# Kernel tuning notes

Measured on AMD Instinct MI355X. Metric: run time of the kernel, lower is better.

## Reference

```python
import jax, jax.numpy as jnp
import numpy as np

B, L, E, H = 4, 1024, 256, 8
DH = E // H  # head_size = 32


def setup_inputs() -> dict:
    key = jax.random.key(0)
    ks = jax.random.split(key, 12)
    node_features = jax.random.normal(ks[0], (B, L, E), dtype=jnp.float32)
    # sparse-ish adjacency with self loops so no row is all-masked
    adj = jax.random.bernoulli(ks[1], 0.05, (B, L, L))
    adj = adj | jnp.eye(L, dtype=bool)[None]
    key_edge_features = jax.random.normal(ks[2], (B, L, L, DH), dtype=jnp.float32)
    s = 1.0 / np.sqrt(E)
    Wq = jax.random.normal(ks[3], (E, E), dtype=jnp.float32) * s
    bq = jnp.zeros((E,), dtype=jnp.float32)
    Wk = jax.random.normal(ks[4], (E, E), dtype=jnp.float32) * s
    bk = jnp.zeros((E,), dtype=jnp.float32)
    Wv = jax.random.normal(ks[5], (E, E), dtype=jnp.float32) * s
    bv = jnp.zeros((E,), dtype=jnp.float32)
    Wo = jax.random.normal(ks[6], (E, E), dtype=jnp.float32) * s
    bo = jnp.zeros((E,), dtype=jnp.float32)
    return {"node_features": node_features, "batched_adj": adj,
            "key_edge_features": key_edge_features,
            "Wq": Wq, "bq": bq, "Wk": Wk, "bk": bk,
            "Wv": Wv, "bv": bv, "Wo": Wo, "bo": bo}


def _heads(x):
    # (B, L, E) -> (B, H, L, DH)
    b, l, _ = x.shape
    return x.reshape(b, l, H, DH).transpose(0, 2, 1, 3)


def reference(node_features, batched_adj, key_edge_features,
              Wq, bq, Wk, bk, Wv, bv, Wo, bo):
    Q = _heads(node_features @ Wq.T + bq)  # (B,H,L,DH)
    K = _heads(node_features @ Wk.T + bk)
    V = _heads(node_features @ Wv.T + bv)
    scores = jnp.einsum('bhnd,bhmd->bhnm', Q, K)
    scores = scores + jnp.einsum('bhnd,bnmd->bhnm', Q, key_edge_features)
    scores = scores / jnp.sqrt(jnp.asarray(E, dtype=scores.dtype))
    adj = batched_adj[:, None, :, :]  # (B,1,L,L) broadcast over heads
    scores = jnp.where(adj, scores, -jnp.inf)
    probs = jax.nn.softmax(scores, axis=-1)
    probs = jnp.where(jnp.isnan(probs), 0.0, probs)  # rows with no edges -> 0
    out = jnp.einsum('bhnm,bhmd->bhnd', probs, V)  # (B,H,L,DH)
    out = out.transpose(0, 2, 1, 3).reshape(node_features.shape[0], -1, E)
    return out @ Wo.T + bo
```

## Files before the change

### kernel.cpp

```cpp
#include <hip/hip_runtime.h>

#define Bv 4
#define Lv 1024
#define Ev 256
#define Hv 8
#define DHv 32

__global__ __launch_bounds__(256) void gemm_fused(
    const float* __restrict__ A,
    const float* __restrict__ W0, const float* __restrict__ b0, float* __restrict__ C0,
    const float* __restrict__ W1, const float* __restrict__ b1, float* __restrict__ C1,
    const float* __restrict__ W2, const float* __restrict__ b2, float* __restrict__ C2) {
    __shared__ float Xs[32][34];
    __shared__ float Ws[32][68];
    const int g = blockIdx.y >> 2;
    const float* __restrict__ W    = (g == 0) ? W0 : (g == 1) ? W1 : W2;
    const float* __restrict__ bias = (g == 0) ? b0 : (g == 1) ? b1 : b2;
    float* __restrict__ C          = (g == 0) ? C0 : (g == 1) ? C1 : C2;

    const int row0 = blockIdx.x * 32;
    const int col0 = (blockIdx.y & 3) * 64;
    const int t = threadIdx.x;
    const int tx = t & 15, ty = t >> 4;
    const int lr = t >> 3, lk = (t & 7) * 4;

    float acc[2][4] = {};

    for (int k0 = 0; k0 < 256; k0 += 32) {
        const float4 av = *(const float4*)&A[(size_t)(row0 + lr) * 256 + k0 + lk];
        const float4 w0 = *(const float4*)&W[(size_t)(col0 + lr) * 256 + k0 + lk];
        const float4 w1 = *(const float4*)&W[(size_t)(col0 + 32 + lr) * 256 + k0 + lk];
        Xs[lk + 0][lr] = av.x; Xs[lk + 1][lr] = av.y;
        Xs[lk + 2][lr] = av.z; Xs[lk + 3][lr] = av.w;
        Ws[lk + 0][lr] = w0.x; Ws[lk + 1][lr] = w0.y;
        Ws[lk + 2][lr] = w0.z; Ws[lk + 3][lr] = w0.w;
        Ws[lk + 0][32 + lr] = w1.x; Ws[lk + 1][32 + lr] = w1.y;
        Ws[lk + 2][32 + lr] = w1.z; Ws[lk + 3][32 + lr] = w1.w;
        __syncthreads();

        #pragma unroll
        for (int kk = 0; kk < 32; ++kk) {
            const float2 a2 = *(const float2*)&Xs[kk][ty * 2];
            const float4 b4 = *(const float4*)&Ws[kk][tx * 4];
            acc[0][0] = fmaf(a2.x, b4.x, acc[0][0]);
            acc[0][1] = fmaf(a2.x, b4.y, acc[0][1]);
            acc[0][2] = fmaf(a2.x, b4.z, acc[0][2]);
            acc[0][3] = fmaf(a2.x, b4.w, acc[0][3]);
            acc[1][0] = fmaf(a2.y, b4.x, acc[1][0]);
            acc[1][1] = fmaf(a2.y, b4.y, acc[1][1]);
            acc[1][2] = fmaf(a2.y, b4.z, acc[1][2]);
            acc[1][3] = fmaf(a2.y, b4.w, acc[1][3]);
        }
        __syncthreads();
    }

    const float4 bv4 = *(const float4*)&bias[col0 + tx * 4];
    #pragma unroll
    for (int ri = 0; ri < 2; ++ri) {
        const int row = row0 + ty * 2 + ri;
        float4 o;
        o.x = acc[ri][0] + bv4.x; o.y = acc[ri][1] + bv4.y;
        o.z = acc[ri][2] + bv4.z; o.w = acc[ri][3] + bv4.w;
        *(float4*)&C[(size_t)row * 256 + col0 + tx * 4] = o;
    }
}

__global__ __launch_bounds__(256) void attn_sparse(const float* __restrict__ Qb,
                                                   const float* __restrict__ Kb,
                                                   const float* __restrict__ Vb,
                                                   const int* __restrict__ adj,
                                                   const float* __restrict__ KE,
                                                   float* __restrict__ AT) {
    __shared__ __align__(16) float Qs[Ev];
    __shared__ __align__(16) float S[Hv][260];
    __shared__ int idxm[256];
    __shared__ int cntS;
    __shared__ float mh[Hv], lh[Hv], scaleh[Hv];

    const int bid = blockIdx.x;
    const int b = bid >> 10;
    const int n = bid & 1023;
    const int t = threadIdx.x;
    const int lane = t & 63;
    const int h_of_t = t >> 5;
    const size_t nrow = (size_t)(b * Lv + n) * Lv;

    Qs[t] = Qb[(size_t)(b * Lv + n) * Ev + t] * 0.0625f;
    if (t < Hv) { mh[t] = -1e30f; lh[t] = 0.f; }

    float acc = 0.f;
    const float* __restrict__ vcol = Vb + (size_t)b * Lv * Ev + t;
    const float4* __restrict__ K4 = (const float4*)Kb;
    const float4* __restrict__ KE4 = (const float4*)KE;
    const float4* __restrict__ Q4 = (const float4*)Qs;

    for (int c = 0; c < 4; ++c) {
        if (t == 0) cntS = 0;
        __syncthreads();

        const int m = c * 256 + t;
        const bool p = adj[nrow + m] != 0;
        const unsigned long long mask = __ballot(p);
        const int prefix = __popcll(mask & ((1ull << lane) - 1ull));
        int base = 0;
        if (lane == 0) base = atomicAdd(&cntS, __popcll(mask));
        base = __shfl(base, 0, 64);
        if (p) idxm[base + prefix] = m;
        __syncthreads();

        const int cnt = cntS;

        for (int tb = 0; tb < cnt * 8; tb += 256) {
            const int task = tb + t;
            if (task < cnt * 8) {
                const int ei = task >> 3, h = task & 7;
                const int mm = idxm[ei];
                const float4* kp = K4 + (size_t)(b * Lv + mm) * 64 + h * 8;
                const float4* kep = KE4 + (nrow + mm) * 8;
                const float4* qp = Q4 + h * 8;
                float dot = 0.f;
                #pragma unroll
                for (int j = 0; j < 8; ++j) {
                    const float4 kv = kp[j], kf = kep[j], qv = qp[j];
                    dot = fmaf(qv.x, kv.x + kf.x, dot);
                    dot = fmaf(qv.y, kv.y + kf.y, dot);
                    dot = fmaf(qv.z, kv.z + kf.z, dot);
                    dot = fmaf(qv.w, kv.w + kf.w, dot);
                }
                S[h][ei] = dot;
            }
        }
        __syncthreads();

        {
            const int h = t >> 5, d = t & 31;
            float cmax = -1e30f;
            for (int i = d; i < cnt; i += 32) cmax = fmaxf(cmax, S[h][i]);
            #pragma unroll
            for (int off = 16; off >= 1; off >>= 1)
                cmax = fmaxf(cmax, __shfl_xor(cmax, off, 64));
            const float oldm = mh[h];
            const float newm = fmaxf(oldm, cmax);
            float csum = 0.f;
            for (int i = d; i < cnt; i += 32) {
                const float pz = __expf(S[h][i] - newm);
                S[h][i] = pz;
                csum += pz;
            }
            #pragma unroll
            for (int off = 16; off >= 1; off >>= 1)
                csum += __shfl_xor(csum, off, 64);
            if (d == 0) {
                const float sc = __expf(oldm - newm);
                scaleh[h] = sc;
                lh[h] = lh[h] * sc + csum;
                mh[h] = newm;
            }
        }
        __syncthreads();

        {
            acc *= scaleh[h_of_t];
            int i = 0;
            for (; i + 4 <= cnt; i += 4) {
                const int m0 = idxm[i], m1 = idxm[i + 1], m2 = idxm[i + 2], m3 = idxm[i + 3];
                const float p0 = S[h_of_t][i],     p1 = S[h_of_t][i + 1];
                const float p2 = S[h_of_t][i + 2], p3 = S[h_of_t][i + 3];
                const float v0 = vcol[(size_t)m0 * Ev];
                const float v1 = vcol[(size_t)m1 * Ev];
                const float v2 = vcol[(size_t)m2 * Ev];
                const float v3 = vcol[(size_t)m3 * Ev];
                acc = fmaf(p0, v0, acc);
                acc = fmaf(p1, v1, acc);
                acc = fmaf(p2, v2, acc);
                acc = fmaf(p3, v3, acc);
            }
            for (; i < cnt; ++i)
                acc = fmaf(S[h_of_t][i], vcol[(size_t)idxm[i] * Ev], acc);
        }
        __syncthreads();
    }

    AT[(size_t)(b * Lv + n) * Ev + t] = acc / lh[h_of_t];
}

extern "C" void kernel_launch(void* const* d_in, const int* in_sizes, int n_in,
                              void* d_out, int out_size, void* d_ws, size_t ws_size,
                              hipStream_t stream) {
    const float* X   = (const float*)d_in[0];
    const int*   adj = (const int*)d_in[1];
    const float* KE  = (const float*)d_in[2];
    const float* Wq  = (const float*)d_in[3];
    const float* bq  = (const float*)d_in[4];
    const float* Wk  = (const float*)d_in[5];
    const float* bk  = (const float*)d_in[6];
    const float* Wv  = (const float*)d_in[7];
    const float* bv  = (const float*)d_in[8];
    const float* Wo  = (const float*)d_in[9];
    const float* bo  = (const float*)d_in[10];

    const size_t NE = (size_t)Bv * Lv * Ev;
    float* Qb = (float*)d_ws;
    float* Kb = Qb + NE;
    float* Vb = Kb + NE;
    float* AT = Vb + NE;
    float* out = (float*)d_out;

    const dim3 blk(256);

    hipLaunchKernelGGL(gemm_fused, dim3(128, 12), blk, 0, stream, X,
                       Wq, bq, Qb, Wk, bk, Kb, Wv, bv, Vb);
    hipLaunchKernelGGL(attn_sparse, dim3(Bv * Lv), blk, 0, stream,
                       Qb, Kb, Vb, adj, KE, AT);
    hipLaunchKernelGGL(gemm_fused, dim3(128, 4), blk, 0, stream, AT,
                       Wo, bo, out, Wo, bo, out, Wo, bo, out);
}
```

Measured before the change: 723.5 us.

## Replace chunked online softmax with single-pass compaction; enlarge GEMM tiles with swizzle

The attention kernel now compacts all neighbours of a row into shared memory up front, then computes scores, an exact softmax and the PV accumulation once. This replaces the four-chunk online-softmax loop and removes most of its barriers and rescaling. Q for each head is held in registers, and each thread keeps a fixed head. The projection GEMM moves to 64x64 tiles with 4x4 per-thread outputs and XOR-swizzled shared stores, so each block does more work per load. The costs are a larger shared-memory footprint (about 37KB per block), which may lower occupancy, and fewer GEMM blocks.

```diff
diff --git a/kernel.cpp b/kernel.cpp
--- a/kernel.cpp
+++ b/kernel.cpp
@@ -11,56 +11,71 @@
     const float* __restrict__ W0, const float* __restrict__ b0, float* __restrict__ C0,
     const float* __restrict__ W1, const float* __restrict__ b1, float* __restrict__ C1,
     const float* __restrict__ W2, const float* __restrict__ b2, float* __restrict__ C2) {
-    __shared__ float Xs[32][34];
+    __shared__ float Xs[32][68];
     __shared__ float Ws[32][68];
     const int g = blockIdx.y >> 2;
     const float* __restrict__ W    = (g == 0) ? W0 : (g == 1) ? W1 : W2;
     const float* __restrict__ bias = (g == 0) ? b0 : (g == 1) ? b1 : b2;
     float* __restrict__ C          = (g == 0) ? C0 : (g == 1) ? C1 : C2;
 
-    const int row0 = blockIdx.x * 32;
+    const int row0 = blockIdx.x * 64;
     const int col0 = (blockIdx.y & 3) * 64;
     const int t = threadIdx.x;
     const int tx = t & 15, ty = t >> 4;
-    const int lr = t >> 3, lk = (t & 7) * 4;
-
-    float acc[2][4] = {};
+    const int lr = t >> 3;
+    const int lk = (t & 7) * 4;
+    const int xsw = 4 * ((lk >> 3) & 3);
+    const int xa = lr ^ xsw;
+
+    float acc[4][4] = {};
 
     for (int k0 = 0; k0 < 256; k0 += 32) {
-        const float4 av = *(const float4*)&A[(size_t)(row0 + lr) * 256 + k0 + lk];
+        const float4 a0 = *(const float4*)&A[(size_t)(row0 + lr) * 256 + k0 + lk];
+        const float4 a1 = *(const float4*)&A[(size_t)(row0 + 32 + lr) * 256 + k0 + lk];
         const float4 w0 = *(const float4*)&W[(size_t)(col0 + lr) * 256 + k0 + lk];
         const float4 w1 = *(const float4*)&W[(size_t)(col0 + 32 + lr) * 256 + k0 + lk];
-        Xs[lk + 0][lr] = av.x; Xs[lk + 1][lr] = av.y;
-        Xs[lk + 2][lr] = av.z; Xs[lk + 3][lr] = av.w;
-        Ws[lk + 0][lr] = w0.x; Ws[lk + 1][lr] = w0.y;
-        Ws[lk + 2][lr] = w0.z; Ws[lk + 3][lr] = w0.w;
-        Ws[lk + 0][32 + lr] = w1.x; Ws[lk + 1][32 + lr] = w1.y;
-        Ws[lk + 2][32 + lr] = w1.z; Ws[lk + 3][32 + lr] = w1.w;
+        Xs[lk + 0][xa] = a0.x; Xs[lk + 1][xa] = a0.y;
+        Xs[lk + 2][xa] = a0.z; Xs[lk + 3][xa] = a0.w;
+        Xs[lk + 0][32 + xa] = a1.x; Xs[lk + 1][32 + xa] = a1.y;
+        Xs[lk + 2][32 + xa] = a1.z; Xs[lk + 3][32 + xa] = a1.w;
+        Ws[lk + 0][xa] = w0.x; Ws[lk + 1][xa] = w0.y;
+        Ws[lk + 2][xa] = w0.z; Ws[lk + 3][xa] = w0.w;
+        Ws[lk + 0][32 + xa] = w1.x; Ws[lk + 1][32 + xa] = w1.y;
+        Ws[lk + 2][32 + xa] = w1.z; Ws[lk + 3][32 + xa] = w1.w;
         __syncthreads();
 
         #pragma unroll
         for (int kk = 0; kk < 32; ++kk) {
-            const float2 a2 = *(const float2*)&Xs[kk][ty * 2];
-            const float4 b4 = *(const float4*)&Ws[kk][tx * 4];
-            acc[0][0] = fmaf(a2.x, b4.x, acc[0][0]);
-            acc[0][1] = fmaf(a2.x, b4.y, acc[0][1]);
-            acc[0][2] = fmaf(a2.x, b4.z, acc[0][2]);
-            acc[0][3] = fmaf(a2.x, b4.w, acc[0][3]);
-            acc[1][0] = fmaf(a2.y, b4.x, acc[1][0]);
-            acc[1][1] = fmaf(a2.y, b4.y, acc[1][1]);
-            acc[1][2] = fmaf(a2.y, b4.z, acc[1][2]);
-            acc[1][3] = fmaf(a2.y, b4.w, acc[1][3]);
+            const int s = (kk >> 3) & 3;
+            const float4 av = *(const float4*)&Xs[kk][(ty ^ s) * 4];
+            const float4 bv = *(const float4*)&Ws[kk][(tx ^ s) * 4];
+            acc[0][0] = fmaf(av.x, bv.x, acc[0][0]);
+            acc[0][1] = fmaf(av.x, bv.y, acc[0][1]);
+            acc[0][2] = fmaf(av.x, bv.z, acc[0][2]);
+            acc[0][3] = fmaf(av.x, bv.w, acc[0][3]);
+            acc[1][0] = fmaf(av.y, bv.x, acc[1][0]);
+            acc[1][1] = fmaf(av.y, bv.y, acc[1][1]);
+            acc[1][2] = fmaf(av.y, bv.z, acc[1][2]);
+            acc[1][3] = fmaf(av.y, bv.w, acc[1][3]);
+            acc[2][0] = fmaf(av.z, bv.x, acc[2][0]);
+            acc[2][1] = fmaf(av.z, bv.y, acc[2][1]);
+            acc[2][2] = fmaf(av.z, bv.z, acc[2][2]);
+            acc[2][3] = fmaf(av.z, bv.w, acc[2][3]);
+            acc[3][0] = fmaf(av.w, bv.x, acc[3][0]);
+            acc[3][1] = fmaf(av.w, bv.y, acc[3][1]);
+            acc[3][2] = fmaf(av.w, bv.z, acc[3][2]);
+            acc[3][3] = fmaf(av.w, bv.w, acc[3][3]);
         }
         __syncthreads();
     }
 
     const float4 bv4 = *(const float4*)&bias[col0 + tx * 4];
     #pragma unroll
-    for (int ri = 0; ri < 2; ++ri) {
-        const int row = row0 + ty * 2 + ri;
+    for (int r = 0; r < 4; ++r) {
+        const int row = row0 + ty * 4 + r;
         float4 o;
-        o.x = acc[ri][0] + bv4.x; o.y = acc[ri][1] + bv4.y;
-        o.z = acc[ri][2] + bv4.z; o.w = acc[ri][3] + bv4.w;
+        o.x = acc[r][0] + bv4.x; o.y = acc[r][1] + bv4.y;
+        o.z = acc[r][2] + bv4.z; o.w = acc[r][3] + bv4.w;
         *(float4*)&C[(size_t)row * 256 + col0 + tx * 4] = o;
     }
 }
@@ -71,117 +86,106 @@
                                                    const int* __restrict__ adj,
                                                    const float* __restrict__ KE,
                                                    float* __restrict__ AT) {
-    __shared__ __align__(16) float Qs[Ev];
-    __shared__ __align__(16) float S[Hv][260];
-    __shared__ int idxm[256];
-    __shared__ int cntS;
-    __shared__ float mh[Hv], lh[Hv], scaleh[Hv];
+    __shared__ float Qs[Hv][36];
+    __shared__ float S[Hv][1028];
+    __shared__ int idxm[Lv];
+    __shared__ int cnt_s;
+    __shared__ float lh[Hv];
 
     const int bid = blockIdx.x;
     const int b = bid >> 10;
     const int n = bid & 1023;
     const int t = threadIdx.x;
     const int lane = t & 63;
-    const int h_of_t = t >> 5;
     const size_t nrow = (size_t)(b * Lv + n) * Lv;
 
-    Qs[t] = Qb[(size_t)(b * Lv + n) * Ev + t] * 0.0625f;
-    if (t < Hv) { mh[t] = -1e30f; lh[t] = 0.f; }
-
-    float acc = 0.f;
-    const float* __restrict__ vcol = Vb + (size_t)b * Lv * Ev + t;
-    const float4* __restrict__ K4 = (const float4*)Kb;
-    const float4* __restrict__ KE4 = (const float4*)KE;
-    const float4* __restrict__ Q4 = (const float4*)Qs;
-
+    Qs[t >> 5][t & 31] = Qb[(size_t)(b * Lv + n) * Ev + t] * 0.0625f;
+    if (t == 0) cnt_s = 0;
+    __syncthreads();
+
+    #pragma unroll
     for (int c = 0; c < 4; ++c) {
-        if (t == 0) cntS = 0;
-        __syncthreads();
-
         const int m = c * 256 + t;
         const bool p = adj[nrow + m] != 0;
         const unsigned long long mask = __ballot(p);
         const int prefix = __popcll(mask & ((1ull << lane) - 1ull));
         int base = 0;
-        if (lane == 0) base = atomicAdd(&cntS, __popcll(mask));
+        if (lane == 0) base = atomicAdd(&cnt_s, __popcll(mask));
         base = __shfl(base, 0, 64);
         if (p) idxm[base + prefix] = m;
-        __syncthreads();
-
-        const int cnt = cntS;
-
-        for (int tb = 0; tb < cnt * 8; tb += 256) {
-            const int task = tb + t;
-            if (task < cnt * 8) {
-                const int ei = task >> 3, h = task & 7;
-                const int mm = idxm[ei];
-                const float4* kp = K4 + (size_t)(b * Lv + mm) * 64 + h * 8;
-                const float4* kep = KE4 + (nrow + mm) * 8;
-                const float4* qp = Q4 + h * 8;
-                float dot = 0.f;
-                #pragma unroll
-                for (int j = 0; j < 8; ++j) {
-                    const float4 kv = kp[j], kf = kep[j], qv = qp[j];
-                    dot = fmaf(qv.x, kv.x + kf.x, dot);
-                    dot = fmaf(qv.y, kv.y + kf.y, dot);
-                    dot = fmaf(qv.z, kv.z + kf.z, dot);
-                    dot = fmaf(qv.w, kv.w + kf.w, dot);
-                }
-                S[h][ei] = dot;
+    }
+    __syncthreads();
+    const int cnt = cnt_s;
+
+    {
+        const int h = t & 7;
+        float4 qf[8];
+        #pragma unroll
+        for (int j = 0; j < 8; ++j) qf[j] = *(const float4*)&Qs[h][j * 4];
+        const float4* __restrict__ K4 = (const float4*)Kb;
+        const float4* __restrict__ KE4 = (const float4*)KE;
+        const int nt = cnt * 8;
+        for (int task = t; task < nt; task += 256) {
+            const int ei = task >> 3;
+            const int mm = idxm[ei];
+            const float4* kp = K4 + (((size_t)(b * Lv + mm)) << 6) + (h << 3);
+            const float4* kep = KE4 + ((nrow + mm) << 3);
+            float dot = 0.f;
+            #pragma unroll
+            for (int j = 0; j < 8; ++j) {
+                const float4 kv = kp[j], kf = kep[j], qv = qf[j];
+                dot = fmaf(qv.x, kv.x + kf.x, dot);
+                dot = fmaf(qv.y, kv.y + kf.y, dot);
+                dot = fmaf(qv.z, kv.z + kf.z, dot);
+                dot = fmaf(qv.w, kv.w + kf.w, dot);
             }
-        }
-        __syncthreads();
-
-        {
-            const int h = t >> 5, d = t & 31;
-            float cmax = -1e30f;
-            for (int i = d; i < cnt; i += 32) cmax = fmaxf(cmax, S[h][i]);
-            #pragma unroll
-            for (int off = 16; off >= 1; off >>= 1)
-                cmax = fmaxf(cmax, __shfl_xor(cmax, off, 64));
-            const float oldm = mh[h];
-            const float newm = fmaxf(oldm, cmax);
-            float csum = 0.f;
-            for (int i = d; i < cnt; i += 32) {
-                const float pz = __expf(S[h][i] - newm);
-                S[h][i] = pz;
-                csum += pz;
-            }
-            #pragma unroll
-            for (int off = 16; off >= 1; off >>= 1)
-                csum += __shfl_xor(csum, off, 64);
-            if (d == 0) {
-                const float sc = __expf(oldm - newm);
-                scaleh[h] = sc;
-                lh[h] = lh[h] * sc + csum;
-                mh[h] = newm;
-            }
-        }
-        __syncthreads();
-
-        {
-            acc *= scaleh[h_of_t];
-            int i = 0;
-            for (; i + 4 <= cnt; i += 4) {
-                const int m0 = idxm[i], m1 = idxm[i + 1], m2 = idxm[i + 2], m3 = idxm[i + 3];
-                const float p0 = S[h_of_t][i],     p1 = S[h_of_t][i + 1];
-                const float p2 = S[h_of_t][i + 2], p3 = S[h_of_t][i + 3];
-                const float v0 = vcol[(size_t)m0 * Ev];
-                const float v1 = vcol[(size_t)m1 * Ev];
-                const float v2 = vcol[(size_t)m2 * Ev];
-                const float v3 = vcol[(size_t)m3 * Ev];
-                acc = fmaf(p0, v0, acc);
-                acc = fmaf(p1, v1, acc);
-                acc = fmaf(p2, v2, acc);
-                acc = fmaf(p3, v3, acc);
-            }
-            for (; i < cnt; ++i)
-                acc = fmaf(S[h_of_t][i], vcol[(size_t)idxm[i] * Ev], acc);
-        }
-        __syncthreads();
-    }
-
-    AT[(size_t)(b * Lv + n) * Ev + t] = acc / lh[h_of_t];
+            S[h][ei] = dot;
+        }
+    }
+    __syncthreads();
+
+    {
+        const int h = t >> 5, d = t & 31;
+        float cmax = -1e30f;
+        for (int i = d; i < cnt; i += 32) cmax = fmaxf(cmax, S[h][i]);
+        #pragma unroll
+        for (int off = 16; off >= 1; off >>= 1)
+            cmax = fmaxf(cmax, __shfl_xor(cmax, off, 64));
+        float csum = 0.f;
+        for (int i = d; i < cnt; i += 32) {
+            const float pz = __expf(S[h][i] - cmax);
+            S[h][i] = pz;
+            csum += pz;
+        }
+        #pragma unroll
+        for (int off = 16; off >= 1; off >>= 1)
+            csum += __shfl_xor(csum, off, 64);
+        if (d == 0) lh[h] = csum;
+    }
+    __syncthreads();
+
+    {
+        const int h = t >> 5;
+        const float* __restrict__ vcol = Vb + (size_t)b * Lv * Ev + t;
+        float acc = 0.f;
+        int i = 0;
+        for (; i + 4 <= cnt; i += 4) {
+            const int m0 = idxm[i], m1 = idxm[i + 1], m2 = idxm[i + 2], m3 = idxm[i + 3];
+            const float p0 = S[h][i],     p1 = S[h][i + 1];
+            const float p2 = S[h][i + 2], p3 = S[h][i + 3];
+            const float v0 = vcol[(size_t)m0 * Ev];
+            const float v1 = vcol[(size_t)m1 * Ev];
+            const float v2 = vcol[(size_t)m2 * Ev];
+            const float v3 = vcol[(size_t)m3 * Ev];
+            acc = fmaf(p0, v0, acc);
+            acc = fmaf(p1, v1, acc);
+            acc = fmaf(p2, v2, acc);
+            acc = fmaf(p3, v3, acc);
+        }
+        for (; i < cnt; ++i)
+            acc = fmaf(S[h][i], vcol[(size_t)idxm[i] * Ev], acc);
+        AT[(size_t)(b * Lv + n) * Ev + t] = acc / lh[h];
+    }
 }
 
 extern "C" void kernel_launch(void* const* d_in, const int* in_sizes, int n_in,
@@ -208,10 +212,10 @@
 
     const dim3 blk(256);
 
-    hipLaunchKernelGGL(gemm_fused, dim3(128, 12), blk, 0, stream, X,
+    hipLaunchKernelGGL(gemm_fused, dim3(64, 12), blk, 0, stream, X,
                        Wq, bq, Qb, Wk, bk, Kb, Wv, bv, Vb);
     hipLaunchKernelGGL(attn_sparse, dim3(Bv * Lv), blk, 0, stream,
                        Qb, Kb, Vb, adj, KE, AT);
-    hipLaunchKernelGGL(gemm_fused, dim3(128, 4), blk, 0, stream, AT,
+    hipLaunchKernelGGL(gemm_fused, dim3(64, 4), blk, 0, stream, AT,
                        Wo, bo, out, Wo, bo, out, Wo, bo, out);
 }
```

New measurement: 726.8 us. No clear change (+0.5%).
